# Kernel tuning notes

Measured on AMD Instinct MI355X. Metric: run time of the kernel, lower is better.

The kernel has to match this reference:

```python
import jax, jax.numpy as jnp
import numpy as np

B, T, E, H = 2048, 128, 192, 192
SCALE = E ** (-0.5)  # original scales by embed_size**-0.5, not head_size


def setup_inputs() -> dict:
    key = jax.random.key(0)
    k1, k2, k3, k4 = jax.random.split(key, 4)
    x = jax.random.normal(k1, (B, T, E), dtype=jnp.float32)
    # torch Linear weights: [out_features, in_features]
    Wq = jax.random.normal(k2, (H, E), dtype=jnp.float32) * (E ** -0.5)
    Wk = jax.random.normal(k3, (H, E), dtype=jnp.float32) * (E ** -0.5)
    Wv = jax.random.normal(k4, (H, E), dtype=jnp.float32) * (E ** -0.5)
    return {"x": x, "Wq": Wq, "Wk": Wk, "Wv": Wv}


def reference(x, Wq, Wk, Wv):
    # projections: y = x @ W.T (torch Linear, no bias)
    q = jnp.einsum("bte,he->bth", x, Wq)
    k = jnp.einsum("bte,he->bth", x, Wk)
    v = jnp.einsum("bte,he->bth", x, Wv)
    wei = jnp.einsum("bqh,bkh->bqk", q, k) * SCALE  # [B,T,T]
    causal = jnp.tril(jnp.ones((T, T), dtype=bool))
    wei = jnp.where(causal, wei, -jnp.inf)
    wei = jax.nn.softmax(wei, axis=-1)
    # dropout omitted: eval-mode (deterministic) reference
    return jnp.einsum("bqk,bkh->bqh", wei, v)
```

## Files before the change

### kernel.cpp

```cpp
#include <hip/hip_runtime.h>
#include <hip/hip_bf16.h>

#define TT 128
#define EE 192
#define HH 192
#define SCALE_F 0.07216878364870322f
#define LOG2E_F 1.4426950408889634f

typedef float f32x4 __attribute__((ext_vector_type(4)));
typedef short short8 __attribute__((ext_vector_type(8)));
typedef short short4v __attribute__((ext_vector_type(4)));

__device__ inline unsigned short f2bf(float x) {
  union { float f; unsigned u; } v; v.f = x;
  unsigned r = v.u + 0x7FFFu + ((v.u >> 16) & 1u);
  return (unsigned short)(r >> 16);
}
__device__ inline unsigned pack2bf(float a, float b) {
  __hip_bfloat162 h = __float22bfloat162_rn(float2{a, b});
  union { __hip_bfloat162 h2; unsigned u; } c; c.h2 = h;
  return c.u;
}

__global__ void pack_wv(const float* __restrict__ Wv, short* __restrict__ out) {
  int f = blockIdx.x * 4 + (threadIdx.x >> 6);
  int lane = threadIdx.x & 63, lg = lane >> 4, lr = lane & 15;
  int tile = f / 6, es = f % 6;
  const float* p = Wv + (16 * tile + lr) * EE + 32 * es + 8 * lg;
  float4 a = *(const float4*)p;
  float4 b = *(const float4*)(p + 4);
  short8 h;
  h[0] = (short)f2bf(a.x); h[1] = (short)f2bf(a.y);
  h[2] = (short)f2bf(a.z); h[3] = (short)f2bf(a.w);
  h[4] = (short)f2bf(b.x); h[5] = (short)f2bf(b.y);
  h[6] = (short)f2bf(b.z); h[7] = (short)f2bf(b.w);
  *(short8*)(out + ((size_t)f * 64 + lane) * 8) = h;
}

__global__ __launch_bounds__(256)
void make_mt(const float* __restrict__ Wq, const float* __restrict__ Wk,
             short* __restrict__ out) {
  __shared__ float red[4][64][8];
  const int f = blockIdx.x;
  const int tid = threadIdx.x;
  const int w = tid >> 6, lane = tid & 63, lg = lane >> 4, lr = lane & 15;
  const int tile = f / 6, es = f % 6;
  const int kcol = 16 * tile + lr;
  const int e1b = 32 * es + 8 * lg;

  float acc[8];
#pragma unroll
  for (int j = 0; j < 8; ++j) acc[j] = 0.f;
#pragma unroll 4
  for (int h = 48 * w; h < 48 * w + 48; ++h) {
    float kv = Wk[h * EE + kcol];
    const float* qp = Wq + h * EE + e1b;
    float4 q0 = *(const float4*)qp, q1 = *(const float4*)(qp + 4);
    acc[0] += q0.x * kv; acc[1] += q0.y * kv;
    acc[2] += q0.z * kv; acc[3] += q0.w * kv;
    acc[4] += q1.x * kv; acc[5] += q1.y * kv;
    acc[6] += q1.z * kv; acc[7] += q1.w * kv;
  }
#pragma unroll
  for (int j = 0; j < 8; ++j) red[w][lane][j] = acc[j];
  __syncthreads();
  if (w == 0) {
    union { unsigned d[4]; short8 s; } h;
#pragma unroll
    for (int i = 0; i < 4; ++i) {
      float a = red[0][lane][2*i]   + red[1][lane][2*i]   + red[2][lane][2*i]   + red[3][lane][2*i];
      float b = red[0][lane][2*i+1] + red[1][lane][2*i+1] + red[2][lane][2*i+1] + red[3][lane][2*i+1];
      h.d[i] = pack2bf(a, b);
    }
    *(short8*)((char*)out + (size_t)f * 1024 + lane * 16) = h.s;
  }
}

__device__ __forceinline__ void proj_v(const char* smem, const short* wfv,
                                       int nt, char* vgb, int mtoff,
                                       int lg, int lr) {
  const f32x4 zero = {0.f, 0.f, 0.f, 0.f};
  const int lane = lg * 16 + lr;
  short8 wg[6];
#pragma unroll
  for (int i = 0; i < 6; ++i)
    wg[i] = *(const short8*)((const char*)wfv + ((size_t)(nt * 6 + i) * 64 + lane) * 16);
#pragma unroll
  for (int mt = 0; mt < 4; ++mt) {
    f32x4 a0 = zero;
#pragma unroll
    for (int es = 0; es < 6; ++es) {
      short8 xf = *(const short8*)(smem + (mt * 6 + es) * 1024 + lane * 16);
      a0 = __builtin_amdgcn_mfma_f32_16x16x32_bf16(xf, wg[es], a0, 0, 0, 0);
    }
    int mtg = mtoff + mt;
    union { unsigned d[2]; short4v v; } pu;
    pu.d[0] = pack2bf(a0[0], a0[1]);
    pu.d[1] = pack2bf(a0[2], a0[3]);
    *(short4v*)(vgb + (size_t)((mtg >> 1) * 12 + nt) * 1024 +
                ((2 * (mtg & 1) + (lg >> 1)) * 16 + lr) * 16 + (lg & 1) * 8) = pu.v;
  }
}

__global__ __launch_bounds__(512)
void v_gemm(const float* __restrict__ x, const short* __restrict__ wfv,
            char* __restrict__ kvws) {
  __shared__ char smem[24576];
  const int bh = blockIdx.x, b = bh >> 1, half = bh & 1;
  const int tid = threadIdx.x;
  const int w = tid >> 6, lane = tid & 63, lg = lane >> 4, lr = lane & 15;
  const float4* xb4 = (const float4*)(x + (size_t)b * (TT * EE) + (size_t)half * 64 * EE);
  char* kvb = kvws + (size_t)b * 98304;

#pragma unroll
  for (int i = 0; i < 6; ++i) {
    int fi = tid + 512 * i;
    int t = fi / 48, c4 = fi % 48;
    float4 f = xb4[fi];
    union { unsigned d[2]; short4v s; } h4;
    h4.d[0] = pack2bf(f.x, f.y);
    h4.d[1] = pack2bf(f.z, f.w);
    int loff = ((t >> 4) * 6 + (c4 >> 3)) * 1024 +
               ((((c4 & 7) >> 1) << 4) + (t & 15)) * 16 + ((c4 & 1) << 3);
    *(short4v*)(smem + loff) = h4.s;
  }
  __syncthreads();

#pragma unroll
  for (int i = 0; i < 3; ++i) {
    int off = (w * 3 + i) * 1024 + lane * 16;
    short8 v = *(const short8*)(smem + off);
    *(short8*)(kvb + (size_t)half * 24576 + off) = v;
  }

  const int mtoff = half * 4;
  char* vgb = kvb + 49152;
  proj_v(smem, wfv, w, vgb, mtoff, lg, lr);
  if (w < 4) proj_v(smem, wfv, 8 + w, vgb, mtoff, lg, lr);
}

__global__ __launch_bounds__(512)
void attn_y(const short* __restrict__ wfy, char* __restrict__ kv) {
  extern __shared__ char smem[];
  char* A = smem;
  char* B = smem + 49152;
  const int b = blockIdx.x;
  const int tid = threadIdx.x;
  const int qt = tid >> 6, lane = tid & 63, lg = lane >> 4, lr = lane & 15;
  const char* xfb = kv + (size_t)b * 98304;
  const char* vb  = xfb + 49152;
  const char* wyc = (const char*)wfy;
  const f32x4 zero = {0.f, 0.f, 0.f, 0.f};

#pragma unroll
  for (int i = 0; i < 6; ++i) {
    int off = (tid + 512 * i) * 16;
    *(short8*)(A + off) = *(const short8*)(xfb + off);
  }
#pragma unroll
  for (int i = 0; i < 9; ++i) {
    int off = (tid + 512 * i) * 16;
    *(short8*)(B + off) = *(const short8*)(wyc + off);
  }
  __syncthreads();

  short8 xfr[6];
#pragma unroll
  for (int i = 0; i < 6; ++i)
    xfr[i] = *(const short8*)(A + (qt * 6 + i) * 1024 + lane * 16);

  unsigned wqp[12][2];
#pragma unroll
  for (int ht = 0; ht < 12; ++ht) {
    f32x4 a = zero;
#pragma unroll
    for (int es = 0; es < 6; ++es) {
      short8 wg = *(const short8*)(B + (ht * 6 + es) * 1024 + lane * 16);
      a = __builtin_amdgcn_mfma_f32_16x16x32_bf16(wg, xfr[es], a, 0, 0, 0);
    }
    wqp[ht][0] = pack2bf(a[0], a[1]);
    wqp[ht][1] = pack2bf(a[2], a[3]);
  }

  short8 qb[6];
#pragma unroll
  for (int ha = 0; ha < 6; ++ha) {
    union { unsigned d[4]; short8 v; } au;
#pragma unroll
    for (int i = 0; i < 4; ++i) {
      int sl = ((2 * (lg & 1) + (i >> 1)) << 4) | lr;
      unsigned v0 = (unsigned)__shfl((int)wqp[2 * ha][i & 1], sl);
      unsigned v1 = (unsigned)__shfl((int)wqp[2 * ha + 1][i & 1], sl);
      au.d[i] = (lg >> 1) ? v1 : v0;
    }
    qb[ha] = au.v;
  }
  __syncthreads();

  short8 vreg[6];
#pragma unroll
  for (int i = 0; i < 6; ++i)
    vreg[i] = *(const short8*)(vb + (qt * 6 + i) * 1024 + lane * 16);

  short8 pa[4];
  {
    f32x4 sa[8];
#pragma unroll
    for (int kt = 0; kt < 8; ++kt) sa[kt] = zero;
#pragma unroll
    for (int kt = 0; kt < 8; ++kt) {
      if (kt <= qt) {
#pragma unroll
        for (int ha = 0; ha < 6; ++ha) {
          short8 ka = *(const short8*)(A + (kt * 6 + ha) * 1024 + lane * 16);
          sa[kt] = __builtin_amdgcn_mfma_f32_16x16x32_bf16(ka, qb[ha], sa[kt], 0, 0, 0);
        }
      }
    }

    const float CSC = SCALE_F * LOG2E_F;
    float m = -INFINITY;
#pragma unroll
    for (int kt = 0; kt < 8; ++kt)
      if (kt <= qt) {
#pragma unroll
        for (int r = 0; r < 4; ++r) {
          float v = sa[kt][r] * CSC;
          if (kt == qt && 4 * lg + r > lr) v = -INFINITY;
          sa[kt][r] = v;
          m = fmaxf(m, v);
        }
      }
    m = fmaxf(m, __shfl_xor(m, 16));
    m = fmaxf(m, __shfl_xor(m, 32));
    float sum = 0.f;
#pragma unroll
    for (int kt = 0; kt < 8; ++kt)
      if (kt <= qt) {
#pragma unroll
        for (int r = 0; r < 4; ++r) {
          float p = exp2f(sa[kt][r] - m);
          sa[kt][r] = p;
          sum += p;
        }
      }
    sum += __shfl_xor(sum, 16);
    sum += __shfl_xor(sum, 32);
    const float rinv = 1.0f / sum;

    unsigned pw[8][2];
#pragma unroll
    for (int kt = 0; kt < 8; ++kt) { pw[kt][0] = 0u; pw[kt][1] = 0u; }
#pragma unroll
    for (int kt = 0; kt < 8; ++kt)
      if (kt <= qt) {
        pw[kt][0] = pack2bf(sa[kt][0] * rinv, sa[kt][1] * rinv);
        pw[kt][1] = pack2bf(sa[kt][2] * rinv, sa[kt][3] * rinv);
      }

#pragma unroll
    for (int tp = 0; tp < 4; ++tp) {
      union { unsigned d[4]; short8 v; } au;
#pragma unroll
      for (int i = 0; i < 4; ++i) {
        int sl = ((2 * (lg & 1) + (i >> 1)) << 4) | lr;
        unsigned lo = (unsigned)__shfl((int)pw[2 * tp][i & 1], sl);
        unsigned hi = (unsigned)__shfl((int)pw[2 * tp + 1][i & 1], sl);
        au.d[i] = (lg >> 1) ? hi : lo;
      }
      pa[tp] = au.v;
    }
  }

#pragma unroll
  for (int i = 0; i < 6; ++i)
    *(short8*)(B + (qt * 6 + i) * 1024 + lane * 16) = vreg[i];
  __syncthreads();

  float* ob = (float*)(kv + (size_t)b * 98304);
#pragma unroll
  for (int half = 0; half < 2; ++half) {
    f32x4 o6[6];
#pragma unroll
    for (int n = 0; n < 6; ++n) o6[n] = zero;
#pragma unroll
    for (int tp = 0; tp < 4; ++tp) {
      if (tp <= (qt >> 1)) {
#pragma unroll
        for (int n = 0; n < 6; ++n) {
          int ht = half * 6 + n;
          short8 va = *(const short8*)(B + (tp * 12 + ht) * 1024 + lane * 16);
          o6[n] = __builtin_amdgcn_mfma_f32_16x16x32_bf16(va, pa[tp], o6[n], 0, 0, 0);
        }
      }
    }
#pragma unroll
    for (int n = 0; n < 6; ++n)
      *(f32x4*)(ob + (16 * qt + lr) * HH + 16 * (half * 6 + n) + 4 * lg) = o6[n];
  }
}

extern "C" void kernel_launch(void* const* d_in, const int* in_sizes, int n_in,
                              void* d_out, int out_size, void* d_ws, size_t ws_size,
                              hipStream_t stream) {
  const float* x  = (const float*)d_in[0];
  const float* Wq = (const float*)d_in[1];
  const float* Wk = (const float*)d_in[2];
  const float* Wv = (const float*)d_in[3];
  int Bn = in_sizes[0] / (TT * EE);

  short* wfy = (short*)d_ws;
  short* wfv = wfy + 36864;

  hipLaunchKernelGGL(pack_wv, dim3(18), dim3(256), 0, stream, Wv, wfv);
  hipLaunchKernelGGL(make_mt, dim3(72), dim3(256), 0, stream, Wq, Wk, wfy);
  hipLaunchKernelGGL(v_gemm, dim3(2 * Bn), dim3(512), 0, stream,
                     x, wfv, (char*)d_out);
  hipLaunchKernelGGL(attn_y, dim3(Bn), dim3(512), 122880, stream,
                     wfy, (char*)d_out);
}
```

Baseline: 194.2 us.

## Fuse V projection into attention kernel, keeping x and V in shared memory

Merges the separate V-GEMM kernel into the attention kernel. Each block now converts x to bf16 in LDS, computes V directly into shared memory, and streams the folded Wq·Wk matrix into a reused LDS buffer in two halves. This removes the global round trip of bf16 x and V through the output buffer and one kernel launch. In exchange it raises LDS use to about 132 KB per block and adds extra barriers, with V projection and weight staging serialized inside each block.

New measurement: 170.9 us. 1.14x faster.

```diff
diff --git a/kernel.cpp b/kernel.cpp
--- a/kernel.cpp
+++ b/kernel.cpp
@@ -76,44 +76,22 @@
   }
 }
 
-__device__ __forceinline__ void proj_v(const char* smem, const short* wfv,
-                                       int nt, char* vgb, int mtoff,
-                                       int lg, int lr) {
+__global__ __launch_bounds__(512)
+void attn_fused(const float* __restrict__ x, const short* __restrict__ wfy,
+                const short* __restrict__ wfv, float* __restrict__ out) {
+  extern __shared__ char smem[];
+  char* A = smem;
+  char* C = smem + 49152;
+  char* D = smem + 98304;
+  const int b = blockIdx.x;
+  const int tid = threadIdx.x;
+  const int qt = tid >> 6, lane = tid & 63, lg = lane >> 4, lr = lane & 15;
+  const float4* xb4 = (const float4*)(x + (size_t)b * (TT * EE));
+  const char* wyc = (const char*)wfy;
   const f32x4 zero = {0.f, 0.f, 0.f, 0.f};
-  const int lane = lg * 16 + lr;
-  short8 wg[6];
-#pragma unroll
-  for (int i = 0; i < 6; ++i)
-    wg[i] = *(const short8*)((const char*)wfv + ((size_t)(nt * 6 + i) * 64 + lane) * 16);
-#pragma unroll
-  for (int mt = 0; mt < 4; ++mt) {
-    f32x4 a0 = zero;
-#pragma unroll
-    for (int es = 0; es < 6; ++es) {
-      short8 xf = *(const short8*)(smem + (mt * 6 + es) * 1024 + lane * 16);
-      a0 = __builtin_amdgcn_mfma_f32_16x16x32_bf16(xf, wg[es], a0, 0, 0, 0);
-    }
-    int mtg = mtoff + mt;
-    union { unsigned d[2]; short4v v; } pu;
-    pu.d[0] = pack2bf(a0[0], a0[1]);
-    pu.d[1] = pack2bf(a0[2], a0[3]);
-    *(short4v*)(vgb + (size_t)((mtg >> 1) * 12 + nt) * 1024 +
-                ((2 * (mtg & 1) + (lg >> 1)) * 16 + lr) * 16 + (lg & 1) * 8) = pu.v;
-  }
-}
-
-__global__ __launch_bounds__(512)
-void v_gemm(const float* __restrict__ x, const short* __restrict__ wfv,
-            char* __restrict__ kvws) {
-  __shared__ char smem[24576];
-  const int bh = blockIdx.x, b = bh >> 1, half = bh & 1;
-  const int tid = threadIdx.x;
-  const int w = tid >> 6, lane = tid & 63, lg = lane >> 4, lr = lane & 15;
-  const float4* xb4 = (const float4*)(x + (size_t)b * (TT * EE) + (size_t)half * 64 * EE);
-  char* kvb = kvws + (size_t)b * 98304;
-
-#pragma unroll
-  for (int i = 0; i < 6; ++i) {
+
+#pragma unroll
+  for (int i = 0; i < 12; ++i) {
     int fi = tid + 512 * i;
     int t = fi / 48, c4 = fi % 48;
     float4 f = xb4[fi];
@@ -122,47 +100,43 @@
     h4.d[1] = pack2bf(f.z, f.w);
     int loff = ((t >> 4) * 6 + (c4 >> 3)) * 1024 +
                ((((c4 & 7) >> 1) << 4) + (t & 15)) * 16 + ((c4 & 1) << 3);
-    *(short4v*)(smem + loff) = h4.s;
+    *(short4v*)(A + loff) = h4.s;
+  }
+#pragma unroll
+  for (int i = 0; i < 5; ++i) {
+    int idx = tid + 512 * i;
+    if (idx < 2304)
+      *(short8*)(D + idx * 16) = *(const short8*)(wyc + (size_t)idx * 16);
   }
   __syncthreads();
 
-#pragma unroll
-  for (int i = 0; i < 3; ++i) {
-    int off = (w * 3 + i) * 1024 + lane * 16;
-    short8 v = *(const short8*)(smem + off);
-    *(short8*)(kvb + (size_t)half * 24576 + off) = v;
-  }
-
-  const int mtoff = half * 4;
-  char* vgb = kvb + 49152;
-  proj_v(smem, wfv, w, vgb, mtoff, lg, lr);
-  if (w < 4) proj_v(smem, wfv, 8 + w, vgb, mtoff, lg, lr);
-}
-
-__global__ __launch_bounds__(512)
-void attn_y(const short* __restrict__ wfy, char* __restrict__ kv) {
-  extern __shared__ char smem[];
-  char* A = smem;
-  char* B = smem + 49152;
-  const int b = blockIdx.x;
-  const int tid = threadIdx.x;
-  const int qt = tid >> 6, lane = tid & 63, lg = lane >> 4, lr = lane & 15;
-  const char* xfb = kv + (size_t)b * 98304;
-  const char* vb  = xfb + 49152;
-  const char* wyc = (const char*)wfy;
-  const f32x4 zero = {0.f, 0.f, 0.f, 0.f};
-
-#pragma unroll
-  for (int i = 0; i < 6; ++i) {
-    int off = (tid + 512 * i) * 16;
-    *(short8*)(A + off) = *(const short8*)(xfb + off);
-  }
-#pragma unroll
-  for (int i = 0; i < 9; ++i) {
-    int off = (tid + 512 * i) * 16;
-    *(short8*)(B + off) = *(const short8*)(wyc + off);
-  }
-  __syncthreads();
+  {
+    const short* wfvp = wfv;
+#pragma unroll
+    for (int u = 0; u < 2; ++u) {
+      int nt = (u == 0) ? qt : (8 + qt);
+      if (u == 1 && qt >= 4) break;
+      short8 wg[6];
+#pragma unroll
+      for (int i = 0; i < 6; ++i)
+        wg[i] = *(const short8*)((const char*)wfvp +
+                 ((size_t)(nt * 6 + i) * 64 + lane) * 16);
+#pragma unroll
+      for (int mt = 0; mt < 8; ++mt) {
+        f32x4 a0 = zero;
+#pragma unroll
+        for (int es = 0; es < 6; ++es) {
+          short8 xf = *(const short8*)(A + (mt * 6 + es) * 1024 + lane * 16);
+          a0 = __builtin_amdgcn_mfma_f32_16x16x32_bf16(xf, wg[es], a0, 0, 0, 0);
+        }
+        union { unsigned d[2]; short4v v; } pu;
+        pu.d[0] = pack2bf(a0[0], a0[1]);
+        pu.d[1] = pack2bf(a0[2], a0[3]);
+        *(short4v*)(C + ((mt >> 1) * 12 + nt) * 1024 +
+                    ((2 * (mt & 1) + (lg >> 1)) * 16 + lr) * 16 + ((lg & 1) << 3)) = pu.v;
+      }
+    }
+  }
 
   short8 xfr[6];
 #pragma unroll
@@ -171,15 +145,37 @@
 
   unsigned wqp[12][2];
 #pragma unroll
-  for (int ht = 0; ht < 12; ++ht) {
+  for (int ht = 0; ht < 6; ++ht) {
     f32x4 a = zero;
 #pragma unroll
     for (int es = 0; es < 6; ++es) {
-      short8 wg = *(const short8*)(B + (ht * 6 + es) * 1024 + lane * 16);
+      short8 wg = *(const short8*)(D + (ht * 6 + es) * 1024 + lane * 16);
       a = __builtin_amdgcn_mfma_f32_16x16x32_bf16(wg, xfr[es], a, 0, 0, 0);
     }
     wqp[ht][0] = pack2bf(a[0], a[1]);
     wqp[ht][1] = pack2bf(a[2], a[3]);
+  }
+  __syncthreads();
+
+#pragma unroll
+  for (int i = 0; i < 5; ++i) {
+    int idx = tid + 512 * i;
+    if (idx < 2304)
+      *(short8*)(D + idx * 16) =
+          *(const short8*)(wyc + 36864 + (size_t)idx * 16);
+  }
+  __syncthreads();
+
+#pragma unroll
+  for (int ht = 0; ht < 6; ++ht) {
+    f32x4 a = zero;
+#pragma unroll
+    for (int es = 0; es < 6; ++es) {
+      short8 wg = *(const short8*)(D + (ht * 6 + es) * 1024 + lane * 16);
+      a = __builtin_amdgcn_mfma_f32_16x16x32_bf16(wg, xfr[es], a, 0, 0, 0);
+    }
+    wqp[6 + ht][0] = pack2bf(a[0], a[1]);
+    wqp[6 + ht][1] = pack2bf(a[2], a[3]);
   }
 
   short8 qb[6];
@@ -195,12 +191,6 @@
     }
     qb[ha] = au.v;
   }
-  __syncthreads();
-
-  short8 vreg[6];
-#pragma unroll
-  for (int i = 0; i < 6; ++i)
-    vreg[i] = *(const short8*)(vb + (qt * 6 + i) * 1024 + lane * 16);
 
   short8 pa[4];
   {
@@ -272,12 +262,7 @@
     }
   }
 
-#pragma unroll
-  for (int i = 0; i < 6; ++i)
-    *(short8*)(B + (qt * 6 + i) * 1024 + lane * 16) = vreg[i];
-  __syncthreads();
-
-  float* ob = (float*)(kv + (size_t)b * 98304);
+  float* ob = out + (size_t)b * (TT * HH);
 #pragma unroll
   for (int half = 0; half < 2; ++half) {
     f32x4 o6[6];
@@ -289,7 +274,7 @@
 #pragma unroll
         for (int n = 0; n < 6; ++n) {
           int ht = half * 6 + n;
-          short8 va = *(const short8*)(B + (tp * 12 + ht) * 1024 + lane * 16);
+          short8 va = *(const short8*)(C + (tp * 12 + ht) * 1024 + lane * 16);
           o6[n] = __builtin_amdgcn_mfma_f32_16x16x32_bf16(va, pa[tp], o6[n], 0, 0, 0);
         }
       }
@@ -314,8 +299,6 @@
 
   hipLaunchKernelGGL(pack_wv, dim3(18), dim3(256), 0, stream, Wv, wfv);
   hipLaunchKernelGGL(make_mt, dim3(72), dim3(256), 0, stream, Wq, Wk, wfy);
-  hipLaunchKernelGGL(v_gemm, dim3(2 * Bn), dim3(512), 0, stream,
-                     x, wfv, (char*)d_out);
-  hipLaunchKernelGGL(attn_y, dim3(Bn), dim3(512), 122880, stream,
-                     wfy, (char*)d_out);
-}
+  hipLaunchKernelGGL(attn_fused, dim3(Bn), dim3(512), 135168, stream,
+                     x, wfy, wfv, (float*)d_out);
+}
```
